# Kernel tuning notes

Measured on AMD Instinct MI355X. Metric: run time of the kernel, lower is better.

Reference implementation:

```python
import jax, jax.numpy as jnp
import numpy as np
import math

C = 512          # in_planes
H = 8            # num_heads
D = C // H       # head_dim = 64
EPS = 1e-12      # torch F.normalize eps


def _l2norm(x):
    # F.normalize(x, dim=-1): x / max(||x||_2, eps)
    n = jnp.sqrt(jnp.sum(x * x, axis=-1, keepdims=True))
    return x / jnp.maximum(n, EPS)


def setup_inputs() -> dict:
    key = jax.random.key(0)
    ks = jax.random.split(key, 8)
    q = jax.random.normal(ks[0], (8, 8, 256, C), dtype=jnp.float32)
    kv = jax.random.normal(ks[1], (8, 8, 512, C), dtype=jnp.float32)
    s = 0.02
    Wq = jax.random.normal(ks[2], (C, C), dtype=jnp.float32) * s
    bq = jax.random.normal(ks[3], (C,), dtype=jnp.float32) * s
    Wkv = jax.random.normal(ks[4], (2 * C, C), dtype=jnp.float32) * s
    bkv = jax.random.normal(ks[5], (2 * C,), dtype=jnp.float32) * s
    Wm = jax.random.normal(ks[6], (C, C), dtype=jnp.float32) * s
    bm = jax.random.normal(ks[7], (C,), dtype=jnp.float32) * s
    return {"q": q, "kv": kv, "Wq": Wq, "bq": bq, "Wkv": Wkv, "bkv": bkv, "Wm": Wm, "bm": bm}


def reference(q, kv, Wq, bq, Wkv, bkv, Wm, bm):
    b, t, lq, c = q.shape
    lk = kv.shape[2]
    shortcut = q

    # Q projection -> (b,t,h,lq,d), L2-normalized over d
    qh = (q @ Wq.T + bq).reshape(b, t, lq, H, D)
    qh = _l2norm(jnp.moveaxis(qh, 3, 2))  # (b,t,h,lq,d)

    # KV projection -> (b,t,2h,lk,d); first H heads = k, last H = v
    kvh = (kv @ Wkv.T + bkv).reshape(b, t, lk, 2 * H, D)
    kvh = jnp.moveaxis(kvh, 3, 2)          # (b,t,2h,lk,d)
    kh = _l2norm(kvh[:, :, :H])            # (b,t,h,lk,d)
    vh = _l2norm(kvh[:, :, H:])            # (b,t,h,lk,d)

    # cosine attention
    att = jnp.einsum('bthqd,bthkd->bthqk', qh, kh) / math.sqrt(D)
    att = jax.nn.softmax(att, axis=-1)
    x = jnp.einsum('bthqk,bthkd->bthqd', att, vh)  # (b,t,h,lq,d)

    # merge heads, output projection, residual
    x = jnp.moveaxis(x, 2, 3).reshape(b, t, lq, c)
    return x @ Wm.T + bm + shortcut
```

## Files before the change

kernel.cpp:

```cpp
#include <hip/hip_runtime.h>
#include <hip/hip_bf16.h>

using bf = __bf16;
typedef __attribute__((ext_vector_type(8))) __bf16 bf16x8;
typedef __attribute__((ext_vector_type(4))) float f32x4;

#define MFMA(a, b, c) __builtin_amdgcn_mfma_f32_16x16x32_bf16((a), (b), (c), 0, 0, 0)
#define GLL16(g, s)                                                         \
    __builtin_amdgcn_global_load_lds(                                       \
        (const __attribute__((address_space(1))) void*)(g),                 \
        (__attribute__((address_space(3))) void*)(s), 16, 0, 0)

static __device__ __forceinline__ void cvt_one(const float* __restrict__ s,
                                               bf* __restrict__ d, int i)
{
    const f32x4 a = ((const f32x4*)s)[2 * i];
    const f32x4 b = ((const f32x4*)s)[2 * i + 1];
    bf16x8 r;
#pragma unroll
    for (int k = 0; k < 4; ++k) { r[k] = (bf)a[k]; r[4 + k] = (bf)b[k]; }
    ((bf16x8*)d)[i] = r;
}

__global__ __launch_bounds__(256) void cvt3(const float* __restrict__ s1, bf* __restrict__ d1, int n1,
                                            const float* __restrict__ s2, bf* __restrict__ d2, int n2,
                                            const float* __restrict__ s3, bf* __restrict__ d3, int n3)
{
    int i = blockIdx.x * 256 + threadIdx.x;
    if (i < n1) { cvt_one(s1, d1, i); return; }
    i -= n1;
    if (i < n2) { cvt_one(s2, d2, i); return; }
    i -= n2;
    if (i < n3) cvt_one(s3, d3, i);
}

template <int EPI, int GH, int LGR, int AF32>
__global__ __launch_bounds__(256) void gemm128(
    const void* __restrict__ Ap, const bf* __restrict__ W,
    const float* __restrict__ bias, const float* __restrict__ res,
    void* __restrict__ Cout, int M, int N, int K)
{
    __shared__ __attribute__((aligned(16))) bf As[128 * 32];
    __shared__ __attribute__((aligned(16))) bf Bs[128 * 32];

    const int lane = threadIdx.x & 63;
    const int wave = threadIdx.x >> 6;
    const int lm = lane & 15;
    const int quad = lane >> 4;
    const int row0 = blockIdx.x * 128, col0 = blockIdx.y * 128;
    const int wrow = (wave >> 1) * 64, wcol = (wave & 1) * 64;

    const int sr = lane >> 2;
    const int sc = (lane & 3) * 8;
    const bf* Ag = nullptr;
    const float* Agf = nullptr;
    if (AF32) Agf = (const float*)Ap + (size_t)(row0 + wave * 32 + sr) * K + sc;
    else      Ag  = (const bf*)Ap + (size_t)(row0 + wave * 32 + sr) * K + sc;
    const bf* Wg = W + (size_t)(col0 + wave * 32 + sr) * K + sc;
    bf* AsW = As + wave * 1024;
    bf* BsW = Bs + wave * 1024;

    f32x4 acc[4][4] = {};

    for (int k0 = 0; k0 < K; k0 += 32) {
        if (AF32) {
            f32x4 u0 = *(const f32x4*)(Agf + k0);
            f32x4 u1 = *(const f32x4*)(Agf + k0 + 4);
            f32x4 u2 = *(const f32x4*)(Agf + (size_t)16 * K + k0);
            f32x4 u3 = *(const f32x4*)(Agf + (size_t)16 * K + k0 + 4);
            bf16x8 r0, r1;
#pragma unroll
            for (int e = 0; e < 4; ++e) {
                r0[e] = (bf)u0[e]; r0[4 + e] = (bf)u1[e];
                r1[e] = (bf)u2[e]; r1[4 + e] = (bf)u3[e];
            }
            *(bf16x8*)(AsW + lane * 8) = r0;
            *(bf16x8*)(AsW + 512 + lane * 8) = r1;
        } else {
            GLL16(Ag + k0, AsW);
            GLL16(Ag + (size_t)16 * K + k0, AsW + 512);
        }
        GLL16(Wg + k0, BsW);
        GLL16(Wg + (size_t)16 * K + k0, BsW + 512);
        __syncthreads();

        bf16x8 a[4], b[4];
#pragma unroll
        for (int i = 0; i < 4; ++i)
            a[i] = *(const bf16x8*)(As + (wrow + i * 16 + lm) * 32 + quad * 8);
#pragma unroll
        for (int j = 0; j < 4; ++j)
            b[j] = *(const bf16x8*)(Bs + (wcol + j * 16 + lm) * 32 + quad * 8);
#pragma unroll
        for (int i = 0; i < 4; ++i)
#pragma unroll
            for (int j = 0; j < 4; ++j)
                acc[i][j] = MFMA(a[i], b[j], acc[i][j]);
        __syncthreads();
    }

    float bv[4];
#pragma unroll
    for (int j = 0; j < 4; ++j) bv[j] = bias[col0 + wcol + j * 16 + lm];

    if (EPI == 0) {
        bf* C = (bf*)Cout;
        const int g = (col0 + wcol) >> 6;
#pragma unroll
        for (int i = 0; i < 4; ++i) {
#pragma unroll
            for (int rg = 0; rg < 4; ++rg) {
                float v[4];
                float ss = 0.f;
#pragma unroll
                for (int j = 0; j < 4; ++j) {
                    const float x = acc[i][j][rg] + bv[j];
                    v[j] = x;
                    ss += x * x;
                }
                ss += __shfl_xor(ss, 1, 64);
                ss += __shfl_xor(ss, 2, 64);
                ss += __shfl_xor(ss, 4, 64);
                ss += __shfl_xor(ss, 8, 64);
                const float inv = 1.0f / fmaxf(sqrtf(ss), 1e-12f);
                const int row = row0 + wrow + i * 16 + quad * 4 + rg;
                const int bt = row >> LGR;
                const int rl = row & ((1 << LGR) - 1);
                bf* Cr = C + (((size_t)(bt * GH + g) << LGR) + rl) * 64;
#pragma unroll
                for (int j = 0; j < 4; ++j)
                    Cr[j * 16 + lm] = (bf)(v[j] * inv);
            }
        }
    } else {
        float* C = (float*)Cout;
#pragma unroll
        for (int i = 0; i < 4; ++i) {
#pragma unroll
            for (int rg = 0; rg < 4; ++rg) {
                const int row = row0 + wrow + i * 16 + quad * 4 + rg;
#pragma unroll
                for (int j = 0; j < 4; ++j) {
                    const size_t idx = (size_t)row * N + col0 + wcol + j * 16 + lm;
                    C[idx] = acc[i][j][rg] + bv[j] + res[idx];
                }
            }
        }
    }
}

template <int GH, int LGR, int AF32>
static __device__ __forceinline__ void gemm256_body(
    const void* __restrict__ Ap, const bf* __restrict__ W,
    const float* __restrict__ bias, bf* __restrict__ C,
    const int bxx, const int byy, const int K)
{
    extern __shared__ __attribute__((aligned(16))) char smem[];
    char* Asm = smem;
    char* Bsm = smem + 65536;

    const int tid = threadIdx.x;
    const int lane = tid & 63;
    const int lm = lane & 15;
    const int quad = lane >> 4;
    const int wave = tid >> 6;
    const int wm = wave >> 2;
    const int wn = wave & 3;
    const int row0 = bxx * 256, col0 = byy * 256;
    const int NT = K >> 6;

    const int trow = tid >> 3;
    const int slotL = tid & 7;
    const int sswz = slotL ^ (trow & 7);
    const float* Af = (const float*)Ap + (size_t)(row0 + trow) * K + slotL * 8;
    const bf*    Ab = (const bf*)Ap + (size_t)(row0 + trow) * K + sswz * 8;
    const bf*    Wth = W + (size_t)(col0 + trow) * K + sswz * 8;

    const char* aBase = Asm + wm * 16384 + lm * 128;
    const char* bBase = Bsm + (wn >> 1) * 16384 + ((wn & 1) * 64 + lm) * 128;
    const int skz0 = ((quad ^ (lm & 7)) << 4);
    const int skz1 = (((4 + quad) ^ (lm & 7)) << 4);

    f32x4 acc[8][4] = {};
    f32x4 areg[4][2];

    auto ldA = [&](int kt) {
#pragma unroll
        for (int hs = 0; hs < 4; ++hs) {
            const float* p = Af + (size_t)((hs >> 1) * 128 + (hs & 1) * 64) * K + kt * 64;
            areg[hs][0] = ((const f32x4*)p)[0];
            areg[hs][1] = ((const f32x4*)p)[1];
        }
    };
    auto wrA = [&](int kt) {
        const int bo = (kt & 1) * 32768;
#pragma unroll
        for (int hs = 0; hs < 4; ++hs) {
            bf16x8 r;
#pragma unroll
            for (int e = 0; e < 4; ++e) {
                r[e] = (bf)areg[hs][0][e];
                r[4 + e] = (bf)areg[hs][1][e];
            }
            *(bf16x8*)(Asm + bo + (hs >> 1) * 16384 + (hs & 1) * 8192 + trow * 128 + sswz * 16) = r;
        }
    };
    auto stAg = [&](int kt) {
        const int bo = (kt & 1) * 32768;
#pragma unroll
        for (int h = 0; h < 2; ++h)
#pragma unroll
            for (int s = 0; s < 2; ++s)
                GLL16(Ab + (size_t)(h * 128 + s * 64) * K + kt * 64,
                      Asm + bo + h * 16384 + s * 8192 + tid * 16);
    };
    auto stB = [&](int kt) {
        const int bo = (kt & 1) * 32768;
#pragma unroll
        for (int h = 0; h < 2; ++h)
#pragma unroll
            for (int s = 0; s < 2; ++s)
                GLL16(Wth + (size_t)(h * 128 + s * 64) * K + kt * 64,
                      Bsm + bo + h * 16384 + s * 8192 + tid * 16);
    };

#define LOADA(bo, mh, kk)                                                     \
    _Pragma("unroll")                                                         \
    for (int mm = 0; mm < 4; ++mm)                                            \
        a[mm] = *(const bf16x8*)(aBase + (bo) + ((mh) * 4 + mm) * 2048        \
                                 + ((kk) ? skz1 : skz0));
#define LOADB(bo, kk)                                                         \
    _Pragma("unroll")                                                         \
    for (int j = 0; j < 4; ++j)                                               \
        b[j] = *(const bf16x8*)(bBase + (bo) + j * 2048                       \
                                + ((kk) ? skz1 : skz0));
#define PH_OPEN()                                                             \
    __builtin_amdgcn_s_barrier();                                             \
    asm volatile("s_waitcnt lgkmcnt(0)" ::: "memory");                        \
    __builtin_amdgcn_s_setprio(1)
#define MM16(mh)                                                              \
    _Pragma("unroll")                                                         \
    for (int mm = 0; mm < 4; ++mm)                                            \
        _Pragma("unroll")                                                     \
        for (int j = 0; j < 4; ++j)                                           \
            acc[(mh) * 4 + mm][j] = MFMA(a[mm], b[j], acc[(mh) * 4 + mm][j]);
#define PH_CLOSE()                                                            \
    __builtin_amdgcn_s_setprio(0);                                            \
    __builtin_amdgcn_s_barrier()

    if (AF32) {
        stB(0); ldA(0); stB(1);
        asm volatile("s_waitcnt vmcnt(4)" ::: "memory");
        wrA(0);
        asm volatile("s_waitcnt lgkmcnt(0)" ::: "memory");
    } else {
        stB(0); stAg(0); stB(1);
        asm volatile("s_waitcnt vmcnt(4)" ::: "memory");
    }
    __builtin_amdgcn_s_barrier();

    for (int it = 0; it < NT; it += 2) {
        const int more = (it + 2 < NT);
        bf16x8 a[4], b[4];

        LOADA(0, 0, 0) LOADB(0, 0)
        if (AF32) ldA(it + 1); else stAg(it + 1);
        PH_OPEN(); MM16(0) PH_CLOSE();

        LOADA(0, 1, 0)
        PH_OPEN(); MM16(1) PH_CLOSE();

        LOADA(0, 0, 1) LOADB(0, 1)
        PH_OPEN(); MM16(0) PH_CLOSE();

        LOADA(0, 1, 1) if (more) stB(it + 2);
        PH_OPEN(); MM16(1)
        __builtin_amdgcn_s_setprio(0);
        if (more) { asm volatile("s_waitcnt vmcnt(4)" ::: "memory"); }
        else      { asm volatile("s_waitcnt vmcnt(0)" ::: "memory"); }
        if (AF32) {
            wrA(it + 1);
            asm volatile("s_waitcnt lgkmcnt(0)" ::: "memory");
        }
        __builtin_amdgcn_s_barrier();

        LOADA(32768, 0, 0) LOADB(32768, 0)
        if (more) { if (AF32) ldA(it + 2); else stAg(it + 2); }
        PH_OPEN(); MM16(0) PH_CLOSE();

        LOADA(32768, 1, 0)
        PH_OPEN(); MM16(1) PH_CLOSE();

        LOADA(32768, 0, 1) LOADB(32768, 1)
        PH_OPEN(); MM16(0) PH_CLOSE();

        LOADA(32768, 1, 1) if (more) stB(it + 3);
        PH_OPEN(); MM16(1)
        __builtin_amdgcn_s_setprio(0);
        if (more) {
            asm volatile("s_waitcnt vmcnt(4)" ::: "memory");
            if (AF32) {
                wrA(it + 2);
                asm volatile("s_waitcnt lgkmcnt(0)" ::: "memory");
            }
        }
        __builtin_amdgcn_s_barrier();
    }
#undef LOADA
#undef LOADB
#undef PH_OPEN
#undef MM16
#undef PH_CLOSE

    float bv[4];
#pragma unroll
    for (int j = 0; j < 4; ++j) bv[j] = bias[col0 + wn * 64 + j * 16 + lm];
    const int g = (col0 + wn * 64) >> 6;
#pragma unroll
    for (int m = 0; m < 8; ++m) {
#pragma unroll
        for (int rg = 0; rg < 4; ++rg) {
            float v[4];
            float ss = 0.f;
#pragma unroll
            for (int j = 0; j < 4; ++j) {
                const float x = acc[m][j][rg] + bv[j];
                v[j] = x;
                ss += x * x;
            }
            ss += __shfl_xor(ss, 1, 64);
            ss += __shfl_xor(ss, 2, 64);
            ss += __shfl_xor(ss, 4, 64);
            ss += __shfl_xor(ss, 8, 64);
            const float inv = 1.0f / fmaxf(sqrtf(ss), 1e-12f);
            const int row = row0 + wm * 128 + m * 16 + quad * 4 + rg;
            const int bt = row >> LGR;
            const int rl = row & ((1 << LGR) - 1);
            bf* Cr = C + (((size_t)(bt * GH + g) << LGR) + rl) * 64;
#pragma unroll
            for (int j = 0; j < 4; ++j)
                Cr[j * 16 + lm] = (bf)(v[j] * inv);
        }
    }
}

__global__ __launch_bounds__(512, 2) void fusedproj(
    const bf* __restrict__ kvb, const bf* __restrict__ wkvb,
    const float* __restrict__ bkv, bf* __restrict__ kvn,
    const float* __restrict__ q, const bf* __restrict__ wqb,
    const float* __restrict__ bq, bf* __restrict__ qn)
{
    const int bx = blockIdx.x;
    if (bx < 128) {
        gemm256_body<8, 8, 1>((const void*)q, wqb, bq, qn, bx & 63, bx >> 6, 512);
    } else {
        const int b2 = bx - 128;
        gemm256_body<16, 9, 0>((const void*)kvb, wkvb, bkv, kvn, b2 & 127, b2 >> 7, 512);
    }
}

__global__ __launch_bounds__(256, 4) void attn(
    const bf* __restrict__ qn, const bf* __restrict__ kvn, bf* __restrict__ X,
    const float* __restrict__ Wm, bf* __restrict__ wmb)
{
    if (blockIdx.x >= 1024) {
        const int t = (blockIdx.x - 1024) * 256 + threadIdx.x;
#pragma unroll 4
        for (int u = t; u < 32768; u += 1024) cvt_one(Wm, wmb, u);
        return;
    }

    __shared__ __attribute__((aligned(16))) bf Kt[128 * 72];
    __shared__ __attribute__((aligned(16))) bf Vt[64 * 136];
    __shared__ __attribute__((aligned(16))) bf Ps[4][16 * 40];

    const int qb = blockIdx.x >> 9;
    const int rb = blockIdx.x & 511;
    const int bt = rb >> 3;
    const int h = rb & 7;
    const int tid = threadIdx.x;
    const int lane = tid & 63;
    const int wave = tid >> 6;
    const int lm = lane & 15;
    const int quad = lane >> 4;

    const bf* qh = qn + ((size_t)(bt * 8 + h) * 256 + qb * 128) * 64;
    const bf* kh = kvn + (size_t)(bt * 16 + h) * 512 * 64;
    const bf* vh = kvn + (size_t)(bt * 16 + 8 + h) * 512 * 64;

    const int srow = tid >> 1;
    const int sseg = (tid & 1) * 32;

    f32x4 o[2][4] = {};
    float sum[2][4] = {};
    bf* Pw = &Ps[wave][0];

    for (int t = 0; t < 4; ++t) {
        {
            const bf* kr = kh + (size_t)(t * 128 + srow) * 64 + sseg;
            bf* kd = Kt + srow * 72 + sseg;
#pragma unroll
            for (int j = 0; j < 4; ++j)
                *(bf16x8*)(kd + j * 8) = *(const bf16x8*)(kr + j * 8);

            const bf* vr = vh + (size_t)(t * 128 + srow) * 64 + sseg;
            bf16x8 vv[4];
#pragma unroll
            for (int j = 0; j < 4; ++j) vv[j] = *(const bf16x8*)(vr + j * 8);
#pragma unroll
            for (int j = 0; j < 4; ++j)
#pragma unroll
                for (int e = 0; e < 8; ++e)
                    Vt[(sseg + j * 8 + e) * 136 + srow] = vv[j][e];
        }
        __syncthreads();

#pragma unroll
        for (int c = 0; c < 2; ++c) {
            const int r0 = wave * 32 + c * 16;
            const bf* qp = qh + (size_t)(r0 + lm) * 64 + quad * 8;
            const bf16x8 a0 = *(const bf16x8*)qp;
            const bf16x8 a1 = *(const bf16x8*)(qp + 32);

            f32x4 s[8];
#pragma unroll
            for (int nt = 0; nt < 8; ++nt) {
                const bf16x8 k0 = *(const bf16x8*)(&Kt[(nt * 16 + lm) * 72 + quad * 8]);
                const bf16x8 k1 = *(const bf16x8*)(&Kt[(nt * 16 + lm) * 72 + 32 + quad * 8]);
                f32x4 z = {};
                z = MFMA(a0, k0, z);
                s[nt] = MFMA(a1, k1, z);
            }

            for (int ntp = 0; ntp < 4; ++ntp) {
#pragma unroll
                for (int tt = 0; tt < 2; ++tt)
#pragma unroll
                    for (int rr = 0; rr < 4; ++rr) {
                        const float e = __expf(s[ntp * 2 + tt][rr] * 0.125f);
                        sum[c][rr] += e;
                        Pw[(quad * 4 + rr) * 40 + tt * 16 + lm] = (bf)e;
                    }
                const bf16x8 ap = *(const bf16x8*)(&Pw[lm * 40 + quad * 8]);
#pragma unroll
                for (int dt = 0; dt < 4; ++dt) {
                    const bf16x8 bv = *(const bf16x8*)(&Vt[(dt * 16 + lm) * 136 + ntp * 32 + quad * 8]);
                    o[c][dt] = MFMA(ap, bv, o[c][dt]);
                }
            }
        }
        __syncthreads();
    }

#pragma unroll
    for (int c = 0; c < 2; ++c) {
        float inv[4];
#pragma unroll
        for (int rr = 0; rr < 4; ++rr) {
            float sm = sum[c][rr];
            sm += __shfl_xor(sm, 1, 64);
            sm += __shfl_xor(sm, 2, 64);
            sm += __shfl_xor(sm, 4, 64);
            sm += __shfl_xor(sm, 8, 64);
            inv[rr] = 1.0f / sm;
        }
        bf* Xp = X + ((size_t)bt * 256 + qb * 128 + wave * 32 + c * 16) * 512 + h * 64;
#pragma unroll
        for (int dt = 0; dt < 4; ++dt)
#pragma unroll
            for (int rr = 0; rr < 4; ++rr)
                Xp[(size_t)(quad * 4 + rr) * 512 + dt * 16 + lm] = (bf)(o[c][dt][rr] * inv[rr]);
    }
}

extern "C" void kernel_launch(void* const* d_in, const int* in_sizes, int n_in,
                              void* d_out, int out_size, void* d_ws, size_t ws_size,
                              hipStream_t stream)
{
    const float* q   = (const float*)d_in[0];
    const float* kv  = (const float*)d_in[1];
    const float* Wq  = (const float*)d_in[2];
    const float* bq  = (const float*)d_in[3];
    const float* Wkv = (const float*)d_in[4];
    const float* bkv = (const float*)d_in[5];
    const float* Wm  = (const float*)d_in[6];
    const float* bm  = (const float*)d_in[7];
    float* out = (float*)d_out;

    char* ws = (char*)d_ws;
    bf* kvb = (bf*)ws;
    bf* kvn = (bf*)(ws + ((size_t)32 << 20));
    bf* X   = (bf*)ws;
    bf* wmb = (bf*)(ws + ((size_t)16 << 20));
    char* dob = (char*)d_out;
    bf* wkvb = (bf*)dob;
    bf* wqb  = (bf*)(dob + ((size_t)1 << 20));
    bf* qn   = (bf*)(dob + ((size_t)16 << 20));

    (void)hipFuncSetAttribute((const void*)fusedproj,
                              hipFuncAttributeMaxDynamicSharedMemorySize, 131072);

    cvt3<<<dim3(8576), 256, 0, stream>>>(kv, kvb, 2097152, Wkv, wkvb, 65536, Wq, wqb, 32768);
    fusedproj<<<dim3(640), 512, 131072, stream>>>(kvb, wkvb, bkv, kvn, q, wqb, bq, qn);
    attn<<<dim3(1028), 256, 0, stream>>>(qn, kvn, X, Wm, wmb);
    gemm128<1, 0, 0, 0><<<dim3(128, 4), 256, 0, stream>>>(X, wmb, bm, q, out, 16384, 512, 512);
}
```

Measured before the change: 292.7 us.

## Merge all stages into one cooperative persistent kernel with grid syncs

Replaces the four launches (conversion, fused projection, attention, output GEMM) with a single cooperative kernel of 256 blocks separated by grid-wide barriers. The projection GEMM tiles are pulled from an atomic job counter. Attention runs two 256-thread halves per block, and the output projection becomes a 256x256-tile GEMM that converts the fp32 Wm weights to bf16 inline. The aim is to remove launch gaps and inter-kernel tails, at the cost of grid.sync overhead, a final phase that uses only 128 of the 256 blocks, and occupancy fixed by cooperative-launch limits.

```diff
diff --git a/kernel.cpp b/kernel.cpp
--- a/kernel.cpp
+++ b/kernel.cpp
@@ -1,5 +1,8 @@
 #include <hip/hip_runtime.h>
 #include <hip/hip_bf16.h>
+#include <hip/hip_cooperative_groups.h>
+
+namespace cg = cooperative_groups;
 
 using bf = __bf16;
 typedef __attribute__((ext_vector_type(8))) __bf16 bf16x8;
@@ -21,208 +24,6 @@
     for (int k = 0; k < 4; ++k) { r[k] = (bf)a[k]; r[4 + k] = (bf)b[k]; }
     ((bf16x8*)d)[i] = r;
 }
-
-__global__ __launch_bounds__(256) void cvt3(const float* __restrict__ s1, bf* __restrict__ d1, int n1,
-                                            const float* __restrict__ s2, bf* __restrict__ d2, int n2,
-                                            const float* __restrict__ s3, bf* __restrict__ d3, int n3)
-{
-    int i = blockIdx.x * 256 + threadIdx.x;
-    if (i < n1) { cvt_one(s1, d1, i); return; }
-    i -= n1;
-    if (i < n2) { cvt_one(s2, d2, i); return; }
-    i -= n2;
-    if (i < n3) cvt_one(s3, d3, i);
-}
-
-template <int EPI, int GH, int LGR, int AF32>
-__global__ __launch_bounds__(256) void gemm128(
-    const void* __restrict__ Ap, const bf* __restrict__ W,
-    const float* __restrict__ bias, const float* __restrict__ res,
-    void* __restrict__ Cout, int M, int N, int K)
-{
-    __shared__ __attribute__((aligned(16))) bf As[128 * 32];
-    __shared__ __attribute__((aligned(16))) bf Bs[128 * 32];
-
-    const int lane = threadIdx.x & 63;
-    const int wave = threadIdx.x >> 6;
-    const int lm = lane & 15;
-    const int quad = lane >> 4;
-    const int row0 = blockIdx.x * 128, col0 = blockIdx.y * 128;
-    const int wrow = (wave >> 1) * 64, wcol = (wave & 1) * 64;
-
-    const int sr = lane >> 2;
-    const int sc = (lane & 3) * 8;
-    const bf* Ag = nullptr;
-    const float* Agf = nullptr;
-    if (AF32) Agf = (const float*)Ap + (size_t)(row0 + wave * 32 + sr) * K + sc;
-    else      Ag  = (const bf*)Ap + (size_t)(row0 + wave * 32 + sr) * K + sc;
-    const bf* Wg = W + (size_t)(col0 + wave * 32 + sr) * K + sc;
-    bf* AsW = As + wave * 1024;
-    bf* BsW = Bs + wave * 1024;
-
-    f32x4 acc[4][4] = {};
-
-    for (int k0 = 0; k0 < K; k0 += 32) {
-        if (AF32) {
-            f32x4 u0 = *(const f32x4*)(Agf + k0);
-            f32x4 u1 = *(const f32x4*)(Agf + k0 + 4);
-            f32x4 u2 = *(const f32x4*)(Agf + (size_t)16 * K + k0);
-            f32x4 u3 = *(const f32x4*)(Agf + (size_t)16 * K + k0 + 4);
-            bf16x8 r0, r1;
-#pragma unroll
-            for (int e = 0; e < 4; ++e) {
-                r0[e] = (bf)u0[e]; r0[4 + e] = (bf)u1[e];
-                r1[e] = (bf)u2[e]; r1[4 + e] = (bf)u3[e];
-            }
-            *(bf16x8*)(AsW + lane * 8) = r0;
-            *(bf16x8*)(AsW + 512 + lane * 8) = r1;
-        } else {
-            GLL16(Ag + k0, AsW);
-            GLL16(Ag + (size_t)16 * K + k0, AsW + 512);
-        }
-        GLL16(Wg + k0, BsW);
-        GLL16(Wg + (size_t)16 * K + k0, BsW + 512);
-        __syncthreads();
-
-        bf16x8 a[4], b[4];
-#pragma unroll
-        for (int i = 0; i < 4; ++i)
-            a[i] = *(const bf16x8*)(As + (wrow + i * 16 + lm) * 32 + quad * 8);
-#pragma unroll
-        for (int j = 0; j < 4; ++j)
-            b[j] = *(const bf16x8*)(Bs + (wcol + j * 16 + lm) * 32 + quad * 8);
-#pragma unroll
-        for (int i = 0; i < 4; ++i)
-#pragma unroll
-            for (int j = 0; j < 4; ++j)
-                acc[i][j] = MFMA(a[i], b[j], acc[i][j]);
-        __syncthreads();
-    }
-
-    float bv[4];
-#pragma unroll
-    for (int j = 0; j < 4; ++j) bv[j] = bias[col0 + wcol + j * 16 + lm];
-
-    if (EPI == 0) {
-        bf* C = (bf*)Cout;
-        const int g = (col0 + wcol) >> 6;
-#pragma unroll
-        for (int i = 0; i < 4; ++i) {
-#pragma unroll
-            for (int rg = 0; rg < 4; ++rg) {
-                float v[4];
-                float ss = 0.f;
-#pragma unroll
-                for (int j = 0; j < 4; ++j) {
-                    const float x = acc[i][j][rg] + bv[j];
-                    v[j] = x;
-                    ss += x * x;
-                }
-                ss += __shfl_xor(ss, 1, 64);
-                ss += __shfl_xor(ss, 2, 64);
-                ss += __shfl_xor(ss, 4, 64);
-                ss += __shfl_xor(ss, 8, 64);
-                const float inv = 1.0f / fmaxf(sqrtf(ss), 1e-12f);
-                const int row = row0 + wrow + i * 16 + quad * 4 + rg;
-                const int bt = row >> LGR;
-                const int rl = row & ((1 << LGR) - 1);
-                bf* Cr = C + (((size_t)(bt * GH + g) << LGR) + rl) * 64;
-#pragma unroll
-                for (int j = 0; j < 4; ++j)
-                    Cr[j * 16 + lm] = (bf)(v[j] * inv);
-            }
-        }
-    } else {
-        float* C = (float*)Cout;
-#pragma unroll
-        for (int i = 0; i < 4; ++i) {
-#pragma unroll
-            for (int rg = 0; rg < 4; ++rg) {
-                const int row = row0 + wrow + i * 16 + quad * 4 + rg;
-#pragma unroll
-                for (int j = 0; j < 4; ++j) {
-                    const size_t idx = (size_t)row * N + col0 + wcol + j * 16 + lm;
-                    C[idx] = acc[i][j][rg] + bv[j] + res[idx];
-                }
-            }
-        }
-    }
-}
-
-template <int GH, int LGR, int AF32>
-static __device__ __forceinline__ void gemm256_body(
-    const void* __restrict__ Ap, const bf* __restrict__ W,
-    const float* __restrict__ bias, bf* __restrict__ C,
-    const int bxx, const int byy, const int K)
-{
-    extern __shared__ __attribute__((aligned(16))) char smem[];
-    char* Asm = smem;
-    char* Bsm = smem + 65536;
-
-    const int tid = threadIdx.x;
-    const int lane = tid & 63;
-    const int lm = lane & 15;
-    const int quad = lane >> 4;
-    const int wave = tid >> 6;
-    const int wm = wave >> 2;
-    const int wn = wave & 3;
-    const int row0 = bxx * 256, col0 = byy * 256;
-    const int NT = K >> 6;
-
-    const int trow = tid >> 3;
-    const int slotL = tid & 7;
-    const int sswz = slotL ^ (trow & 7);
-    const float* Af = (const float*)Ap + (size_t)(row0 + trow) * K + slotL * 8;
-    const bf*    Ab = (const bf*)Ap + (size_t)(row0 + trow) * K + sswz * 8;
-    const bf*    Wth = W + (size_t)(col0 + trow) * K + sswz * 8;
-
-    const char* aBase = Asm + wm * 16384 + lm * 128;
-    const char* bBase = Bsm + (wn >> 1) * 16384 + ((wn & 1) * 64 + lm) * 128;
-    const int skz0 = ((quad ^ (lm & 7)) << 4);
-    const int skz1 = (((4 + quad) ^ (lm & 7)) << 4);
-
-    f32x4 acc[8][4] = {};
-    f32x4 areg[4][2];
-
-    auto ldA = [&](int kt) {
-#pragma unroll
-        for (int hs = 0; hs < 4; ++hs) {
-            const float* p = Af + (size_t)((hs >> 1) * 128 + (hs & 1) * 64) * K + kt * 64;
-            areg[hs][0] = ((const f32x4*)p)[0];
-            areg[hs][1] = ((const f32x4*)p)[1];
-        }
-    };
-    auto wrA = [&](int kt) {
-        const int bo = (kt & 1) * 32768;
-#pragma unroll
-        for (int hs = 0; hs < 4; ++hs) {
-            bf16x8 r;
-#pragma unroll
-            for (int e = 0; e < 4; ++e) {
-                r[e] = (bf)areg[hs][0][e];
-                r[4 + e] = (bf)areg[hs][1][e];
-            }
-            *(bf16x8*)(Asm + bo + (hs >> 1) * 16384 + (hs & 1) * 8192 + trow * 128 + sswz * 16) = r;
-        }
-    };
-    auto stAg = [&](int kt) {
-        const int bo = (kt & 1) * 32768;
-#pragma unroll
-        for (int h = 0; h < 2; ++h)
-#pragma unroll
-            for (int s = 0; s < 2; ++s)
-                GLL16(Ab + (size_t)(h * 128 + s * 64) * K + kt * 64,
-                      Asm + bo + h * 16384 + s * 8192 + tid * 16);
-    };
-    auto stB = [&](int kt) {
-        const int bo = (kt & 1) * 32768;
-#pragma unroll
-        for (int h = 0; h < 2; ++h)
-#pragma unroll
-            for (int s = 0; s < 2; ++s)
-                GLL16(Wth + (size_t)(h * 128 + s * 64) * K + kt * 64,
-                      Bsm + bo + h * 16384 + s * 8192 + tid * 16);
-    };
 
 #define LOADA(bo, mh, kk)                                                     \
     _Pragma("unroll")                                                         \
@@ -248,6 +49,81 @@
     __builtin_amdgcn_s_setprio(0);                                            \
     __builtin_amdgcn_s_barrier()
 
+template <int GH, int LGR, int AF32>
+static __device__ __forceinline__ void gemm256_body(
+    const void* __restrict__ Ap, const bf* __restrict__ W,
+    const float* __restrict__ bias, bf* __restrict__ C,
+    const int bxx, const int byy, const int K)
+{
+    extern __shared__ __attribute__((aligned(16))) char smem[];
+    char* Asm = smem;
+    char* Bsm = smem + 65536;
+
+    const int tid = threadIdx.x;
+    const int lane = tid & 63;
+    const int lm = lane & 15;
+    const int quad = lane >> 4;
+    const int wave = tid >> 6;
+    const int wm = wave >> 2;
+    const int wn = wave & 3;
+    const int row0 = bxx * 256, col0 = byy * 256;
+    const int NT = K >> 6;
+
+    const int trow = tid >> 3;
+    const int slotL = tid & 7;
+    const int sswz = slotL ^ (trow & 7);
+    const float* Af = (const float*)Ap + (size_t)(row0 + trow) * K + slotL * 8;
+    const bf*    Ab = (const bf*)Ap + (size_t)(row0 + trow) * K + sswz * 8;
+    const bf*    Wth = W + (size_t)(col0 + trow) * K + sswz * 8;
+
+    const char* aBase = Asm + wm * 16384 + lm * 128;
+    const char* bBase = Bsm + (wn >> 1) * 16384 + ((wn & 1) * 64 + lm) * 128;
+    const int skz0 = ((quad ^ (lm & 7)) << 4);
+    const int skz1 = (((4 + quad) ^ (lm & 7)) << 4);
+
+    f32x4 acc[8][4] = {};
+    f32x4 areg[4][2];
+
+    auto ldA = [&](int kt) {
+#pragma unroll
+        for (int hs = 0; hs < 4; ++hs) {
+            const float* p = Af + (size_t)((hs >> 1) * 128 + (hs & 1) * 64) * K + kt * 64;
+            areg[hs][0] = ((const f32x4*)p)[0];
+            areg[hs][1] = ((const f32x4*)p)[1];
+        }
+    };
+    auto wrA = [&](int kt) {
+        const int bo = (kt & 1) * 32768;
+#pragma unroll
+        for (int hs = 0; hs < 4; ++hs) {
+            bf16x8 r;
+#pragma unroll
+            for (int e = 0; e < 4; ++e) {
+                r[e] = (bf)areg[hs][0][e];
+                r[4 + e] = (bf)areg[hs][1][e];
+            }
+            *(bf16x8*)(Asm + bo + (hs >> 1) * 16384 + (hs & 1) * 8192 + trow * 128 + sswz * 16) = r;
+        }
+    };
+    auto stAg = [&](int kt) {
+        const int bo = (kt & 1) * 32768;
+#pragma unroll
+        for (int h = 0; h < 2; ++h)
+#pragma unroll
+            for (int s = 0; s < 2; ++s)
+                GLL16(Ab + (size_t)(h * 128 + s * 64) * K + kt * 64,
+                      Asm + bo + h * 16384 + s * 8192 + tid * 16);
+    };
+    auto stB = [&](int kt) {
+        const int bo = (kt & 1) * 32768;
+#pragma unroll
+        for (int h = 0; h < 2; ++h)
+#pragma unroll
+            for (int s = 0; s < 2; ++s)
+                GLL16(Wth + (size_t)(h * 128 + s * 64) * K + kt * 64,
+                      Bsm + bo + h * 16384 + s * 8192 + tid * 16);
+    };
+
     if (AF32) {
         stB(0); ldA(0); stB(1);
         asm volatile("s_waitcnt vmcnt(4)" ::: "memory");
@@ -306,11 +182,6 @@
         }
         __builtin_amdgcn_s_barrier();
     }
-#undef LOADA
-#undef LOADB
-#undef PH_OPEN
-#undef MM16
-#undef PH_CLOSE
 
     float bv[4];
 #pragma unroll
@@ -344,41 +215,131 @@
     }
 }
 
-__global__ __launch_bounds__(512, 2) void fusedproj(
-    const bf* __restrict__ kvb, const bf* __restrict__ wkvb,
-    const float* __restrict__ bkv, bf* __restrict__ kvn,
-    const float* __restrict__ q, const bf* __restrict__ wqb,
-    const float* __restrict__ bq, bf* __restrict__ qn)
+static __device__ __forceinline__ void gemm256_out_body(
+    const bf* __restrict__ Xin, const float* __restrict__ Wm,
+    const float* __restrict__ bm, const float* __restrict__ res,
+    float* __restrict__ out, const int bxx, const int byy)
 {
-    const int bx = blockIdx.x;
-    if (bx < 128) {
-        gemm256_body<8, 8, 1>((const void*)q, wqb, bq, qn, bx & 63, bx >> 6, 512);
-    } else {
-        const int b2 = bx - 128;
-        gemm256_body<16, 9, 0>((const void*)kvb, wkvb, bkv, kvn, b2 & 127, b2 >> 7, 512);
+    extern __shared__ __attribute__((aligned(16))) char smem[];
+    char* Asm = smem;
+    char* Bsm = smem + 65536;
+    const int K = 512, N = 512, NT = 8;
+
+    const int tid = threadIdx.x;
+    const int lane = tid & 63;
+    const int lm = lane & 15;
+    const int quad = lane >> 4;
+    const int wave = tid >> 6;
+    const int wm = wave >> 2;
+    const int wn = wave & 3;
+    const int row0 = bxx * 256, col0 = byy * 256;
+
+    const int trow = tid >> 3;
+    const int slotL = tid & 7;
+    const int sswz = slotL ^ (trow & 7);
+    const bf* Ab = Xin + (size_t)(row0 + trow) * K + sswz * 8;
+    const float* Wf = Wm + (size_t)(col0 + trow) * K + slotL * 8;
+
+    const char* aBase = Asm + wm * 16384 + lm * 128;
+    const char* bBase = Bsm + (wn >> 1) * 16384 + ((wn & 1) * 64 + lm) * 128;
+    const int skz0 = ((quad ^ (lm & 7)) << 4);
+    const int skz1 = (((4 + quad) ^ (lm & 7)) << 4);
+
+    f32x4 acc[8][4] = {};
+    f32x4 breg[4][2];
+
+    auto stA = [&](int kt) {
+        const int bo = (kt & 1) * 32768;
+#pragma unroll
+        for (int h = 0; h < 2; ++h)
+#pragma unroll
+            for (int s = 0; s < 2; ++s)
+                GLL16(Ab + (size_t)(h * 128 + s * 64) * K + kt * 64,
+                      Asm + bo + h * 16384 + s * 8192 + tid * 16);
+    };
+    auto ldB = [&](int kt) {
+#pragma unroll
+        for (int hs = 0; hs < 4; ++hs) {
+            const float* p = Wf + (size_t)((hs >> 1) * 128 + (hs & 1) * 64) * K + kt * 64;
+            breg[hs][0] = ((const f32x4*)p)[0];
+            breg[hs][1] = ((const f32x4*)p)[1];
+        }
+    };
+    auto wrB = [&](int kt) {
+        const int bo = (kt & 1) * 32768;
+#pragma unroll
+        for (int hs = 0; hs < 4; ++hs) {
+            bf16x8 r;
+#pragma unroll
+            for (int e = 0; e < 4; ++e) {
+                r[e] = (bf)breg[hs][0][e];
+                r[4 + e] = (bf)breg[hs][1][e];
+            }
+            *(bf16x8*)(Bsm + bo + (hs >> 1) * 16384 + (hs & 1) * 8192 + trow * 128 + sswz * 16) = r;
+        }
+    };
+
+    stA(0); ldB(0);
+    asm volatile("s_waitcnt vmcnt(0)" ::: "memory");
+    wrB(0);
+    asm volatile("s_waitcnt lgkmcnt(0)" ::: "memory");
+    __builtin_amdgcn_s_barrier();
+
+    for (int it = 0; it < NT; ++it) {
+        const int more = (it + 1 < NT);
+        const int bo = (it & 1) * 32768;
+        bf16x8 a[4], b[4];
+
+        LOADA(bo, 0, 0) LOADB(bo, 0)
+        if (more) { stA(it + 1); ldB(it + 1); }
+        PH_OPEN(); MM16(0) PH_CLOSE();
+
+        LOADA(bo, 1, 0)
+        PH_OPEN(); MM16(1) PH_CLOSE();
+
+        LOADA(bo, 0, 1) LOADB(bo, 1)
+        PH_OPEN(); MM16(0) PH_CLOSE();
+
+        LOADA(bo, 1, 1)
+        PH_OPEN(); MM16(1)
+        __builtin_amdgcn_s_setprio(0);
+        if (more) {
+            asm volatile("s_waitcnt vmcnt(0)" ::: "memory");
+            wrB(it + 1);
+            asm volatile("s_waitcnt lgkmcnt(0)" ::: "memory");
+        }
+        __builtin_amdgcn_s_barrier();
+    }
+
+    float bv[4];
+#pragma unroll
+    for (int j = 0; j < 4; ++j) bv[j] = bm[col0 + wn * 64 + j * 16 + lm];
+#pragma unroll
+    for (int m = 0; m < 8; ++m) {
+#pragma unroll
+        for (int rg = 0; rg < 4; ++rg) {
+            const int row = row0 + wm * 128 + m * 16 + quad * 4 + rg;
+#pragma unroll
+            for (int j = 0; j < 4; ++j) {
+                const size_t idx = (size_t)row * N + col0 + wn * 64 + j * 16 + lm;
+                out[idx] = acc[m][j][rg] + bv[j] + res[idx];
+            }
+        }
     }
 }
 
-__global__ __launch_bounds__(256, 4) void attn(
+static __device__ __forceinline__ void attn_unit(
     const bf* __restrict__ qn, const bf* __restrict__ kvn, bf* __restrict__ X,
-    const float* __restrict__ Wm, bf* __restrict__ wmb)
+    const int u, char* __restrict__ sm, const int tid)
 {
-    if (blockIdx.x >= 1024) {
-        const int t = (blockIdx.x - 1024) * 256 + threadIdx.x;
-#pragma unroll 4
-        for (int u = t; u < 32768; u += 1024) cvt_one(Wm, wmb, u);
-        return;
-    }
-
-    __shared__ __attribute__((aligned(16))) bf Kt[128 * 72];
-    __shared__ __attribute__((aligned(16))) bf Vt[64 * 136];
-    __shared__ __attribute__((aligned(16))) bf Ps[4][16 * 40];
-
-    const int qb = blockIdx.x >> 9;
-    const int rb = blockIdx.x & 511;
+    bf* Kt = (bf*)sm;
+    bf* Vt = (bf*)(sm + 18432);
+    bf* Ps = (bf*)(sm + 35840);
+
+    const int qb = u >> 9;
+    const int rb = u & 511;
     const int bt = rb >> 3;
     const int h = rb & 7;
-    const int tid = threadIdx.x;
     const int lane = tid & 63;
     const int wave = tid >> 6;
     const int lm = lane & 15;
@@ -393,7 +354,7 @@
 
     f32x4 o[2][4] = {};
     float sum[2][4] = {};
-    bf* Pw = &Ps[wave][0];
+    bf* Pw = Ps + wave * 640;
 
     for (int t = 0; t < 4; ++t) {
         {
@@ -457,12 +418,12 @@
         float inv[4];
 #pragma unroll
         for (int rr = 0; rr < 4; ++rr) {
-            float sm = sum[c][rr];
-            sm += __shfl_xor(sm, 1, 64);
-            sm += __shfl_xor(sm, 2, 64);
-            sm += __shfl_xor(sm, 4, 64);
-            sm += __shfl_xor(sm, 8, 64);
-            inv[rr] = 1.0f / sm;
+            float sm2 = sum[c][rr];
+            sm2 += __shfl_xor(sm2, 1, 64);
+            sm2 += __shfl_xor(sm2, 2, 64);
+            sm2 += __shfl_xor(sm2, 4, 64);
+            sm2 += __shfl_xor(sm2, 8, 64);
+            inv[rr] = 1.0f / sm2;
         }
         bf* Xp = X + ((size_t)bt * 256 + qb * 128 + wave * 32 + c * 16) * 512 + h * 64;
 #pragma unroll
@@ -472,6 +433,72 @@
                 Xp[(size_t)(quad * 4 + rr) * 512 + dt * 16 + lm] = (bf)(o[c][dt][rr] * inv[rr]);
     }
 }
+
+__global__ __launch_bounds__(512, 2) void mega(
+    const float* __restrict__ q, const float* __restrict__ kv,
+    const float* __restrict__ Wq, const float* __restrict__ bq,
+    const float* __restrict__ Wkv, const float* __restrict__ bkv,
+    const float* __restrict__ Wm, const float* __restrict__ bm,
+    float* __restrict__ out,
+    bf* __restrict__ kvb, bf* __restrict__ kvn, bf* __restrict__ X,
+    bf* __restrict__ qn, bf* __restrict__ wkvb, bf* __restrict__ wqb,
+    unsigned* __restrict__ ctr)
+{
+    cg::grid_group grid = cg::this_grid();
+    const int bid = blockIdx.x;
+    const int tid = threadIdx.x;
+
+    if (bid == 0 && tid == 0) *ctr = 0u;
+    {
+        const int idx = bid * 512 + tid;
+        for (int u = idx; u < 2195456; u += 131072) {
+            if (u < 2097152)       cvt_one(kv, kvb, u);
+            else if (u < 2162688)  cvt_one(Wkv, wkvb, u - 2097152);
+            else                   cvt_one(Wq, wqb, u - 2162688);
+        }
+    }
+    __threadfence();
+    grid.sync();
+
+    {
+        __shared__ int sjob;
+        for (;;) {
+            __syncthreads();
+            if (tid == 0) sjob = (int)atomicAdd(ctr, 1u);
+            __syncthreads();
+            const int j = sjob;
+            if (j >= 640) break;
+            if (j < 128)
+                gemm256_body<8, 8, 1>((const void*)q, wqb, bq, qn, j & 63, j >> 6, 512);
+            else {
+                const int k = j - 128;
+                gemm256_body<16, 9, 0>((const void*)kvb, wkvb, bkv, kvn, k & 127, k >> 7, 512);
+            }
+        }
+    }
+    __threadfence();
+    grid.sync();
+
+    {
+        extern __shared__ __attribute__((aligned(16))) char smem[];
+        const int tid2 = tid & 255;
+        const int half = tid >> 8;
+        char* sm = smem + half * 40960;
+        attn_unit(qn, kvn, X, (bid << 1) | half, sm, tid2);
+        attn_unit(qn, kvn, X, 512 + ((bid << 1) | half), sm, tid2);
+    }
+    __threadfence();
+    grid.sync();
+
+    if (bid < 128)
+        gemm256_out_body(X, Wm, bm, q, out, bid & 63, bid >> 6);
+}
+
+#undef LOADA
+#undef LOADB
+#undef PH_OPEN
+#undef MM16
+#undef PH_CLOSE
 
 extern "C" void kernel_launch(void* const* d_in, const int* in_sizes, int n_in,
                               void* d_out, int out_size, void* d_ws, size_t ws_size,
@@ -491,17 +518,19 @@
     bf* kvb = (bf*)ws;
     bf* kvn = (bf*)(ws + ((size_t)32 << 20));
     bf* X   = (bf*)ws;
-    bf* wmb = (bf*)(ws + ((size_t)16 << 20));
     char* dob = (char*)d_out;
-    bf* wkvb = (bf*)dob;
-    bf* wqb  = (bf*)(dob + ((size_t)1 << 20));
-    bf* qn   = (bf*)(dob + ((size_t)16 << 20));
-
-    (void)hipFuncSetAttribute((const void*)fusedproj,
+    bf* qn   = (bf*)dob;
+    bf* wkvb = (bf*)(dob + ((size_t)16 << 20));
+    bf* wqb  = (bf*)(dob + ((size_t)17 << 20));
+    unsigned* ctr = (unsigned*)(dob + ((size_t)18 << 20));
+
+    (void)hipFuncSetAttribute((const void*)mega,
                               hipFuncAttributeMaxDynamicSharedMemorySize, 131072);
 
-    cvt3<<<dim3(8576), 256, 0, stream>>>(kv, kvb, 2097152, Wkv, wkvb, 65536, Wq, wqb, 32768);
-    fusedproj<<<dim3(640), 512, 131072, stream>>>(kvb, wkvb, bkv, kvn, q, wqb, bq, qn);
-    attn<<<dim3(1028), 256, 0, stream>>>(qn, kvn, X, Wm, wmb);
-    gemm128<1, 0, 0, 0><<<dim3(128, 4), 256, 0, stream>>>(X, wmb, bm, q, out, 16384, 512, 512);
+    void* args[] = { (void*)&q, (void*)&kv, (void*)&Wq, (void*)&bq,
+                     (void*)&Wkv, (void*)&bkv, (void*)&Wm, (void*)&bm,
+                     (void*)&out, (void*)&kvb, (void*)&kvn, (void*)&X,
+                     (void*)&qn, (void*)&wkvb, (void*)&wqb, (void*)&ctr };
+    (void)hipLaunchCooperativeKernel((const void*)mega, dim3(256), dim3(512),
+                                     args, 131072, stream);
 }
```

After: 597.7 us. 2.04x slower.
